# Kernel tuning notes

Hardware: AMD Instinct MI355X
Metric: run time of the kernel (lower is better)

The kernel has to match this reference:

```python
import jax, jax.numpy as jnp
import numpy as np

B, P, K, H, C = 8, 4096, 20, 64, 40  # clouds, points/cloud, knn k, hidden_feat, num_classes
NEG = 0.2  # LeakyReLU negative slope used by the repo MLP


def setup_inputs() -> dict:
    key = jax.random.key(0)
    ks = jax.random.split(key, 16)
    w = lambda k, shape: (jax.random.normal(k, shape, jnp.float32) / np.sqrt(shape[0]))
    return {
        "x": jax.random.normal(ks[0], (B * P, 3), jnp.float32),
        "batch": jnp.repeat(jnp.arange(B, dtype=jnp.int32), P),
        "W1": w(ks[1], (2 * 3, H)), "b1": jnp.zeros((H,), jnp.float32),
        "W2": w(ks[2], (2 * H, H)), "b2": jnp.zeros((H,), jnp.float32),
        "W3": w(ks[3], (2 * H, H)), "b3": jnp.zeros((H,), jnp.float32),
        "Wl": w(ks[4], (3 * H, 1024)), "bl": jnp.zeros((1024,), jnp.float32),
        "Wm1": w(ks[5], (1024, 256)), "bm1": jnp.zeros((256,), jnp.float32),
        "Wm2": w(ks[6], (256, 128)), "bm2": jnp.zeros((128,), jnp.float32),
        "Wo": w(ks[7], (128, C)), "bo": jnp.zeros((C,), jnp.float32),
    }


def _knn_idx(x):
    # x: [B,P,d] -> indices of K nearest neighbors (excluding self): [B,P,K]
    d2 = jnp.sum(x * x, axis=-1)  # [B,P]
    dist = d2[:, :, None] + d2[:, None, :] - 2.0 * jnp.einsum('bpd,bqd->bpq', x, x)
    dist = dist + jnp.eye(x.shape[1], dtype=x.dtype) * 1e10  # mask self-loops
    return jax.lax.top_k(-dist, K)[1]


def _edge_conv(x, W, b):
    # DynamicEdgeConv with max aggregation: nn([x_i, x_j - x_i]) maxed over K neighbors
    idx = _knn_idx(x)                                    # [B,P,K]
    x_j = jax.vmap(lambda xb, ib: xb[ib])(x, idx)        # [B,P,K,d]
    x_i = jnp.broadcast_to(x[:, :, None, :], x_j.shape)  # [B,P,K,d]
    feat = jnp.concatenate([x_i, x_j - x_i], axis=-1)    # [B,P,K,2d]
    h = jax.nn.leaky_relu(feat @ W + b, NEG)             # [B,P,K,H]
    return jnp.max(h, axis=2)                            # [B,P,H]


def reference(x, batch, W1, b1, W2, b2, W3, b3, Wl, bl, Wm1, bm1, Wm2, bm2, Wo, bo):
    # batch is sorted with equal-size clouds -> reshape to [B,P,3]
    xb = x.reshape(B, P, 3)
    x1 = _edge_conv(xb, W1, b1)
    x2 = _edge_conv(x1, W2, b2)
    x3 = _edge_conv(x2, W3, b3)
    h = jnp.concatenate([x1, x2, x3], axis=-1)           # [B,P,3H]
    h = jax.nn.leaky_relu(h @ Wl + bl, NEG)
    h = jax.nn.leaky_relu(h @ Wm1 + bm1, NEG)            # dropout = identity (eval)
    h = jax.nn.leaky_relu(h @ Wm2 + bm2, NEG)
    out = h @ Wo + bo                                    # [B,P,C]
    return jax.nn.log_softmax(out, axis=-1).reshape(B * P, C)
```

## Files before the change

### kernel.cpp

```cpp
#include <hip/hip_runtime.h>
#include <cstddef>
#include <cstdint>

constexpr int B_ = 8, P_ = 4096, K_ = 20, H_ = 64, C_ = 40;
constexpr int NPT = B_ * P_;
#define NEG_SLOPE 0.2f

typedef unsigned long long u64;
typedef unsigned int u32;
typedef unsigned short u16;
typedef __attribute__((ext_vector_type(8))) short bf16x8;
typedef __attribute__((ext_vector_type(4))) float f32x4;

__device__ inline u16 f2bf(float v) {
    u32 bits = __float_as_uint(v);
    return (u16)((bits + 0x7FFFu + ((bits >> 16) & 1)) >> 16);
}
__device__ inline float bf2f(u16 h) { return __uint_as_float((u32)h << 16); }

__device__ __forceinline__ void bubble20f(float (&a)[K_], float key) {
    float carry = key;
#pragma unroll
    for (int s = 0; s < K_; ++s) {
        float as = a[s];
        a[s]  = fminf(carry, as);
        carry = fmaxf(carry, as);
    }
}
__device__ __forceinline__ float mkkey(float dist, int cid) {
    return __uint_as_float((__float_as_uint(dist) & 0xFFFFF000u) | (u32)cid);
}

__global__ __launch_bounds__(256) void pack4_kernel(const float* __restrict__ x,
                                                    float4* __restrict__ xp) {
    int i = blockIdx.x * 256 + threadIdx.x;
    if (i >= NPT) return;
    float ax = x[(size_t)i * 3], ay = x[(size_t)i * 3 + 1], az = x[(size_t)i * 3 + 2];
    xp[i] = make_float4(ax, ay, az, ax * ax + ay * ay + az * az);
}

__global__ __launch_bounds__(256) void d2cvt2_kernel(const float* __restrict__ x,
                                                     float* __restrict__ d2,
                                                     u16* __restrict__ xh,
                                                     u16* __restrict__ xm) {
    int i = blockIdx.x * 256 + threadIdx.x;
    if (i >= NPT) return;
    const float* r = x + (size_t)i * 64;
    float s = 0.f;
#pragma unroll
    for (int d8 = 0; d8 < 64; d8 += 8) {
        float4 v0 = *(const float4*)(r + d8);
        float4 v1 = *(const float4*)(r + d8 + 4);
        s += v0.x * v0.x + v0.y * v0.y + v0.z * v0.z + v0.w * v0.w;
        s += v1.x * v1.x + v1.y * v1.y + v1.z * v1.z + v1.w * v1.w;
        float av[8] = {v0.x, v0.y, v0.z, v0.w, v1.x, v1.y, v1.z, v1.w};
        bf16x8 vh, vm;
#pragma unroll
        for (int j = 0; j < 8; ++j) {
            u16 h = f2bf(av[j]);
            float r1 = av[j] - bf2f(h);
            vh[j] = (short)h; vm[j] = (short)f2bf(r1);
        }
        *(bf16x8*)(xh + (size_t)i * 64 + d8) = vh;
        *(bf16x8*)(xm + (size_t)i * 64 + d8) = vm;
    }
    d2[i] = s;
}

__global__ __launch_bounds__(256) void knnf3_kernel(const float4* __restrict__ xp,
                                                    int* __restrict__ idx) {
    int b = blockIdx.y;
    int q0 = blockIdx.x * 64;
    const float4* xb = xp + (size_t)b * P_;

    int t = threadIdx.x, w = t >> 6, ln = t & 63;
    int q  = ln & 15;
    int ss = ln >> 4;

    int qrow = q0 + w * 16 + q;
    float4 qv = xb[qrow];

    float a[K_];
#pragma unroll
    for (int s = 0; s < K_; ++s)
        a[s] = __uint_as_float(0x7F7FF000u | (u32)s);
    const float PINV = __uint_as_float(0x7F800000u);
    const float BIGF = __uint_as_float(0x7F7FFFFFu);

    float p0 = PINV, p1 = PINV, p2 = PINV, p3 = PINV;
    int pcnt = 0;
    float kthr = BIGF;

#pragma unroll 1
    for (int c0 = 0; c0 < P_; c0 += 64) {
#pragma unroll
        for (int nt = 0; nt < 4; ++nt) {
            float4 cv[4];
#pragma unroll
            for (int r = 0; r < 4; ++r)
                cv[r] = xb[c0 + nt * 16 + ss * 4 + r];
#pragma unroll
            for (int r = 0; r < 4; ++r) {
                int cID = c0 + nt * 16 + ss * 4 + r;
                float dv = (qv.w + cv[r].w)
                         - 2.f * (qv.x * cv[r].x + qv.y * cv[r].y + qv.z * cv[r].z);
                if (cID == qrow) dv += 1e10f;
                dv = fmaxf(dv, 0.f);
                if (__any(dv <= kthr)) {
                    float key = mkkey(dv, cID);
                    bool pass = key < a[K_ - 1];
                    p3 = pass ? p2 : p3;
                    p2 = pass ? p1 : p2;
                    p1 = pass ? p0 : p1;
                    p0 = pass ? key : p0;
                    pcnt = pass ? pcnt + 1 : pcnt;
                    if (__any(pcnt >= 4)) {
                        bubble20f(a, p3); bubble20f(a, p2); bubble20f(a, p1); bubble20f(a, p0);
                        p0 = p1 = p2 = p3 = PINV; pcnt = 0;
                        kthr = __uint_as_float(__float_as_uint(a[K_ - 1]) | 0xFFFu);
                    }
                }
            }
        }
    }
    bubble20f(a, p3); bubble20f(a, p2); bubble20f(a, p1); bubble20f(a, p0);

    int* op = idx + ((size_t)(b * P_ + qrow)) * K_;
#pragma unroll 1
    for (int k = 0; k < K_; ++k) {
        float v = a[0];
        float v1 = __shfl_xor(v, 16);
        v = fminf(v, v1);
        float v2 = __shfl_xor(v, 32);
        v = fminf(v, v2);
        bool win = (__float_as_uint(a[0]) == __float_as_uint(v));
#pragma unroll
        for (int s = 0; s < K_ - 1; ++s) a[s] = win ? a[s + 1] : a[s];
        a[K_ - 1] = win ? BIGF : a[K_ - 1];
        if (ss == 0)
            op[k] = b * P_ + (int)(__float_as_uint(v) & 0xFFFu);
    }
}

__global__ __launch_bounds__(256) void knnm64_kernel(const u16* __restrict__ xh,
                                                     const u16* __restrict__ xm,
                                                     const float* __restrict__ d2,
                                                     int* __restrict__ idx) {
    __shared__ u16 sH[64 * 64];
    __shared__ u16 sM[64 * 64];
    __shared__ float sd2[P_];

    int b = blockIdx.y;
    int q0 = blockIdx.x * 64;
    const u16* xhb = xh + (size_t)b * P_ * 64;
    const u16* xmb = xm + (size_t)b * P_ * 64;
    const float* d2b = d2 + (size_t)b * P_;

    int t = threadIdx.x, w = t >> 6, ln = t & 63;
    int q  = ln & 15;
    int ss = ln >> 4;

    for (int i = t; i < P_ / 4; i += 256)
        ((float4*)sd2)[i] = ((const float4*)d2b)[i];

    int qrow = q0 + w * 16 + q;
    bf16x8 qh[2], qm[2];
#pragma unroll
    for (int kt = 0; kt < 2; ++kt) {
        size_t off = (size_t)qrow * 64 + kt * 32 + ss * 8;
        qh[kt] = *(const bf16x8*)(xhb + off);
        qm[kt] = *(const bf16x8*)(xmb + off);
    }

    __syncthreads();
    float qd2 = sd2[qrow];

    float a[K_];
#pragma unroll
    for (int s = 0; s < K_; ++s)
        a[s] = __uint_as_float(0x7F7FF000u | (u32)s);
    const float PINV = __uint_as_float(0x7F800000u);
    const float BIGF = __uint_as_float(0x7F7FFFFFu);

    float p0 = PINV, p1 = PINV, p2 = PINV, p3 = PINV;
    int pcnt = 0;
    float kthr = BIGF;

    int sr = t >> 2;
    int sk2 = (t & 3) * 32;
    int sbase = sr * 128, sswz = (sr & 7) << 4;
    size_t sgof = (size_t)sr * 64 + (t & 3) * 16;

#pragma unroll 1
    for (int c0 = 0; c0 < P_; c0 += 64) {
        __syncthreads();
        {
            size_t g = (size_t)c0 * 64 + sgof;
            bf16x8 h0 = *(const bf16x8*)(xhb + g);
            bf16x8 h1 = *(const bf16x8*)(xhb + g + 8);
            bf16x8 m0 = *(const bf16x8*)(xmb + g);
            bf16x8 m1 = *(const bf16x8*)(xmb + g + 8);
            *(bf16x8*)((char*)sH + sbase + (sk2 ^ sswz)) = h0;
            *(bf16x8*)((char*)sH + sbase + ((sk2 + 16) ^ sswz)) = h1;
            *(bf16x8*)((char*)sM + sbase + (sk2 ^ sswz)) = m0;
            *(bf16x8*)((char*)sM + sbase + ((sk2 + 16) ^ sswz)) = m1;
        }
        __syncthreads();

        f32x4 acc[4];
#pragma unroll
        for (int nt = 0; nt < 4; ++nt) {
            acc[nt] = (f32x4){0.f, 0.f, 0.f, 0.f};
            int r = nt * 16 + q;
            int base = r * 128, swz = (r & 7) << 4;
#pragma unroll
            for (int kt = 0; kt < 2; ++kt) {
                int k2 = kt * 64 + ss * 16;
                bf16x8 ch = *(const bf16x8*)((char*)sH + base + (k2 ^ swz));
                bf16x8 cm = *(const bf16x8*)((char*)sM + base + (k2 ^ swz));
                acc[nt] = __builtin_amdgcn_mfma_f32_16x16x32_bf16(cm, qh[kt], acc[nt], 0, 0, 0);
                acc[nt] = __builtin_amdgcn_mfma_f32_16x16x32_bf16(ch, qm[kt], acc[nt], 0, 0, 0);
                acc[nt] = __builtin_amdgcn_mfma_f32_16x16x32_bf16(ch, qh[kt], acc[nt], 0, 0, 0);
            }
        }

        float dvv[4][4];
        float mn = 3.4e38f;
#pragma unroll
        for (int nt = 0; nt < 4; ++nt) {
#pragma unroll
            for (int r = 0; r < 4; ++r) {
                int cID = c0 + nt * 16 + ss * 4 + r;
                float dv = (qd2 + sd2[cID]) - 2.f * acc[nt][r];
                if (cID == qrow) dv += 1e10f;
                dv = fmaxf(dv, 0.f);
                dvv[nt][r] = dv;
                mn = fminf(mn, dv);
            }
        }
        if (__any(mn <= kthr)) {
#pragma unroll
            for (int nt = 0; nt < 4; ++nt) {
#pragma unroll
                for (int r = 0; r < 4; ++r) {
                    float dv = dvv[nt][r];
                    if (__any(dv <= kthr)) {
                        float key = mkkey(dv, c0 + nt * 16 + ss * 4 + r);
                        bool pass = key < a[K_ - 1];
                        p3 = pass ? p2 : p3;
                        p2 = pass ? p1 : p2;
                        p1 = pass ? p0 : p1;
                        p0 = pass ? key : p0;
                        pcnt = pass ? pcnt + 1 : pcnt;
                        if (__any(pcnt >= 4)) {
                            bubble20f(a, p3); bubble20f(a, p2); bubble20f(a, p1); bubble20f(a, p0);
                            p0 = p1 = p2 = p3 = PINV; pcnt = 0;
                            kthr = __uint_as_float(__float_as_uint(a[K_ - 1]) | 0xFFFu);
                        }
                    }
                }
            }
        }
    }
    bubble20f(a, p3); bubble20f(a, p2); bubble20f(a, p1); bubble20f(a, p0);

    int* op = idx + ((size_t)(b * P_ + qrow)) * K_;
#pragma unroll 1
    for (int k = 0; k < K_; ++k) {
        float v = a[0];
        float v1 = __shfl_xor(v, 16);
        v = fminf(v, v1);
        float v2 = __shfl_xor(v, 32);
        v = fminf(v, v2);
        bool win = (__float_as_uint(a[0]) == __float_as_uint(v));
#pragma unroll
        for (int s = 0; s < K_ - 1; ++s) a[s] = win ? a[s + 1] : a[s];
        a[K_ - 1] = win ? BIGF : a[K_ - 1];
        if (ss == 0)
            op[k] = b * P_ + (int)(__float_as_uint(v) & 0xFFFu);
    }
}

__global__ __launch_bounds__(256) void prep_kernel(const float* __restrict__ W2,
                                                   const float* __restrict__ b2,
                                                   const float* __restrict__ W3,
                                                   const float* __restrict__ b3,
                                                   const float* __restrict__ Wl,
                                                   const float* __restrict__ Wm1,
                                                   const float* __restrict__ Wm2,
                                                   float* __restrict__ Wpk2, float* __restrict__ bpk2,
                                                   float* __restrict__ Wpk3, float* __restrict__ bpk3,
                                                   u16* __restrict__ WlT,
                                                   u16* __restrict__ Wm1T,
                                                   u16* __restrict__ Wm2T) {
    int t = blockIdx.x * 256 + threadIdx.x;
    if (t < 8192) {
        int d = t >> 7, h2 = t & 127;
        Wpk2[t] = (h2 < 64) ? W2[d * 64 + h2] : W2[(64 + d) * 64 + (h2 - 64)];
        if (t < 128) bpk2[t] = (t < 64) ? b2[t] : 0.f;
    } else if (t < 16384) {
        int t2 = t - 8192;
        int d = t2 >> 7, h2 = t2 & 127;
        Wpk3[t2] = (h2 < 64) ? W3[d * 64 + h2] : W3[(64 + d) * 64 + (h2 - 64)];
        if (t2 < 128) bpk3[t2] = (t2 < 64) ? b3[t2] : 0.f;
    } else if (t < 212992) {
        int t2 = t - 16384;
        int k = t2 >> 10, n = t2 & 1023;
        WlT[(size_t)n * 192 + k] = f2bf(Wl[t2]);
    } else if (t < 475136) {
        int t2 = t - 212992;
        int k = t2 >> 8, n = t2 & 255;
        Wm1T[(size_t)n * 1024 + k] = f2bf(Wm1[t2]);
    } else if (t < 507904) {
        int t2 = t - 475136;
        int k = t2 >> 7, n = t2 & 127;
        Wm2T[(size_t)n * 256 + k] = f2bf(Wm2[t2]);
    }
}

__global__ __launch_bounds__(256) void uv3_kernel(const float* __restrict__ x,
                                                  const float* __restrict__ W,
                                                  const float* __restrict__ b,
                                                  float* __restrict__ UV) {
    int t = blockIdx.x * 256 + threadIdx.x;
    int p = t >> 7, h2 = t & 127;
    float x0 = x[p * 3], x1 = x[p * 3 + 1], x2 = x[p * 3 + 2];
    float r;
    if (h2 < 64) {
        r = b[h2] + x0 * W[h2] + x1 * W[64 + h2] + x2 * W[128 + h2];
    } else {
        int h = h2 - 64;
        r = x0 * W[192 + h] + x1 * W[256 + h] + x2 * W[320 + h];
    }
    UV[t] = r;
}

__global__ __launch_bounds__(256) void edgemax_kernel(const float* __restrict__ UV,
                                                      const int* __restrict__ idx,
                                                      float* __restrict__ xout) {
    int wv = threadIdx.x >> 6, lane = threadIdx.x & 63;
    int p = blockIdx.x * 4 + wv;
    const float* uvp = UV + (size_t)p * 128;
    float duv = uvp[lane] - uvp[64 + lane];
    const int* ip = idx + (size_t)p * K_;
    int jj[K_];
#pragma unroll
    for (int k = 0; k < K_; ++k) jj[k] = ip[k];
    float m = -3.4e38f;
#pragma unroll
    for (int k = 0; k < K_; ++k) {
        float vj = UV[(size_t)jj[k] * 128 + 64 + lane];
        float t = duv + vj;
        m = fmaxf(m, fmaxf(t, NEG_SLOPE * t));
    }
    xout[(size_t)p * H_ + lane] = m;
}

__global__ __launch_bounds__(256) void gemm_kernel(const float* __restrict__ A1,
                                                   const float* __restrict__ Wm,
                                                   const float* __restrict__ bias,
                                                   float* __restrict__ Cm,
                                                   int M, int N, int Kd, int leaky) {
    __shared__ float sA[32][68];
    __shared__ float sB[32][68];

    int tid = threadIdx.x;
    int row0 = blockIdx.x * 64, col0 = blockIdx.y * 64;
    int tx = tid & 15, ty = tid >> 4;

    int lr  = tid >> 2;
    int lk4 = (tid & 3) * 4;
    int lkb = tid >> 4;
    int lnb = (tid & 15) * 4;

    float acc[4][4] = {};

    for (int k0 = 0; k0 < Kd; k0 += 32) {
        int arow = row0 + lr;
#pragma unroll
        for (int h = 0; h < 32; h += 16) {
            int kk = k0 + lk4 + h;
            const float* src = A1 + (size_t)arow * Kd + kk;
            float4 av = *(const float4*)src;
            sA[lk4 + h + 0][lr] = av.x; sA[lk4 + h + 1][lr] = av.y;
            sA[lk4 + h + 2][lr] = av.z; sA[lk4 + h + 3][lr] = av.w;
        }
        int bcol = col0 + lnb;
#pragma unroll
        for (int h = 0; h < 32; h += 16) {
            float4 bv = make_float4(0.f, 0.f, 0.f, 0.f);
            if (bcol < N) bv = *(const float4*)(Wm + (size_t)(k0 + lkb + h) * N + bcol);
            *(float4*)&sB[lkb + h][lnb] = bv;
        }
        __syncthreads();

#pragma unroll
        for (int kk2 = 0; kk2 < 32; ++kk2) {
            float4 a = *(const float4*)&sA[kk2][ty * 4];
            float4 bb = *(const float4*)&sB[kk2][tx * 4];
            acc[0][0] = fmaf(a.x, bb.x, acc[0][0]); acc[0][1] = fmaf(a.x, bb.y, acc[0][1]);
            acc[0][2] = fmaf(a.x, bb.z, acc[0][2]); acc[0][3] = fmaf(a.x, bb.w, acc[0][3]);
            acc[1][0] = fmaf(a.y, bb.x, acc[1][0]); acc[1][1] = fmaf(a.y, bb.y, acc[1][1]);
            acc[1][2] = fmaf(a.y, bb.z, acc[1][2]); acc[1][3] = fmaf(a.y, bb.w, acc[1][3]);
            acc[2][0] = fmaf(a.z, bb.x, acc[2][0]); acc[2][1] = fmaf(a.z, bb.y, acc[2][1]);
            acc[2][2] = fmaf(a.z, bb.z, acc[2][2]); acc[2][3] = fmaf(a.z, bb.w, acc[2][3]);
            acc[3][0] = fmaf(a.w, bb.x, acc[3][0]); acc[3][1] = fmaf(a.w, bb.y, acc[3][1]);
            acc[3][2] = fmaf(a.w, bb.z, acc[3][2]); acc[3][3] = fmaf(a.w, bb.w, acc[3][3]);
        }
        __syncthreads();
    }

    for (int i = 0; i < 4; ++i) {
        int row = row0 + ty * 4 + i;
        for (int j = 0; j < 4; ++j) {
            int col = col0 + tx * 4 + j;
            if (col < N) {
                float v = acc[i][j] + bias[col];
                if (leaky) v = v > 0.f ? v : NEG_SLOPE * v;
                Cm[(size_t)row * N + col] = v;
            }
        }
    }
}

template <int KD, int OUT_BF16>
__global__ __launch_bounds__(256) void gemm_mfma_kernel(const u16* __restrict__ A,
                                                        const u16* __restrict__ BT,
                                                        const float* __restrict__ bias,
                                                        void* __restrict__ Cout,
                                                        int N, int leaky) {
    __shared__ u16 sA[128 * 64];
    __shared__ u16 sB[128 * 64];

    int t = threadIdx.x;
    int wave = t >> 6, lane = t & 63;
    int wm = wave >> 1, wn = wave & 1;
    int row0 = blockIdx.x * 128;
    int col0 = blockIdx.y * 128;

    f32x4 acc[4][4] = {};

    for (int k0 = 0; k0 < KD; k0 += 64) {
        __syncthreads();
#pragma unroll
        for (int i = 0; i < 4; ++i) {
            int li = t + i * 256;
            int r = li >> 3;
            int kc = (li & 7) * 8;
            bf16x8 v = *(const bf16x8*)(A + (size_t)(row0 + r) * KD + k0 + kc);
            *(bf16x8*)((char*)sA + r * 128 + ((kc * 2) ^ ((r & 7) << 4))) = v;
        }
#pragma unroll
        for (int i = 0; i < 4; ++i) {
            int li = t + i * 256;
            int n = li >> 3;
            int kc = (li & 7) * 8;
            bf16x8 v = *(const bf16x8*)(BT + (size_t)(col0 + n) * KD + k0 + kc);
            *(bf16x8*)((char*)sB + n * 128 + ((kc * 2) ^ ((n & 7) << 4))) = v;
        }
        __syncthreads();

#pragma unroll
        for (int kk = 0; kk < 2; ++kk) {
            int kb = kk * 64 + (lane >> 4) * 16;
            bf16x8 af[4], bfr[4];
#pragma unroll
            for (int mi = 0; mi < 4; ++mi) {
                int r = wm * 64 + mi * 16 + (lane & 15);
                af[mi] = *(const bf16x8*)((char*)sA + r * 128 + (kb ^ ((r & 7) << 4)));
            }
#pragma unroll
            for (int ni = 0; ni < 4; ++ni) {
                int n = wn * 64 + ni * 16 + (lane & 15);
                bfr[ni] = *(const bf16x8*)((char*)sB + n * 128 + (kb ^ ((n & 7) << 4)));
            }
#pragma unroll
            for (int mi = 0; mi < 4; ++mi)
#pragma unroll
                for (int ni = 0; ni < 4; ++ni)
                    acc[mi][ni] = __builtin_amdgcn_mfma_f32_16x16x32_bf16(
                        af[mi], bfr[ni], acc[mi][ni], 0, 0, 0);
        }
    }

#pragma unroll
    for (int ni = 0; ni < 4; ++ni) {
        int col = col0 + wn * 64 + ni * 16 + (lane & 15);
        float bs = bias[col];
#pragma unroll
        for (int mi = 0; mi < 4; ++mi) {
#pragma unroll
            for (int r = 0; r < 4; ++r) {
                int row = row0 + wm * 64 + mi * 16 + (lane >> 4) * 4 + r;
                float v = acc[mi][ni][r] + bs;
                if (leaky) v = v > 0.f ? v : NEG_SLOPE * v;
                if (OUT_BF16)
                    ((u16*)Cout)[(size_t)row * N + col] = f2bf(v);
                else
                    ((float*)Cout)[(size_t)row * N + col] = v;
            }
        }
    }
}

__global__ __launch_bounds__(256) void gemm_mfma_cat_kernel(const float* __restrict__ x1,
                                                            const float* __restrict__ x2,
                                                            const float* __restrict__ x3,
                                                            const u16* __restrict__ BT,
                                                            const float* __restrict__ bias,
                                                            u16* __restrict__ Cout,
                                                            int N) {
    __shared__ u16 sA[128 * 64];
    __shared__ u16 sB[128 * 64];

    int t = threadIdx.x;
    int wave = t >> 6, lane = t & 63;
    int wm = wave >> 1, wn = wave & 1;
    int row0 = blockIdx.x * 128;
    int col0 = blockIdx.y * 128;

    f32x4 acc[4][4] = {};

#pragma unroll 1
    for (int k0 = 0; k0 < 192; k0 += 64) {
        const float* src = (k0 == 0) ? x1 : (k0 == 64) ? x2 : x3;
        __syncthreads();
#pragma unroll
        for (int i = 0; i < 4; ++i) {
            int li = t + i * 256;
            int r = li >> 3;
            int kc = (li & 7) * 8;
            const float* sp = src + (size_t)(row0 + r) * 64 + kc;
            float4 a0 = *(const float4*)sp;
            float4 a1 = *(const float4*)(sp + 4);
            bf16x8 v;
            v[0] = (short)f2bf(a0.x); v[1] = (short)f2bf(a0.y);
            v[2] = (short)f2bf(a0.z); v[3] = (short)f2bf(a0.w);
            v[4] = (short)f2bf(a1.x); v[5] = (short)f2bf(a1.y);
            v[6] = (short)f2bf(a1.z); v[7] = (short)f2bf(a1.w);
            *(bf16x8*)((char*)sA + r * 128 + ((kc * 2) ^ ((r & 7) << 4))) = v;
        }
#pragma unroll
        for (int i = 0; i < 4; ++i) {
            int li = t + i * 256;
            int n = li >> 3;
            int kc = (li & 7) * 8;
            bf16x8 v = *(const bf16x8*)(BT + (size_t)(col0 + n) * 192 + k0 + kc);
            *(bf16x8*)((char*)sB + n * 128 + ((kc * 2) ^ ((n & 7) << 4))) = v;
        }
        __syncthreads();

#pragma unroll
        for (int kk = 0; kk < 2; ++kk) {
            int kb = kk * 64 + (lane >> 4) * 16;
            bf16x8 af[4], bfr[4];
#pragma unroll
            for (int mi = 0; mi < 4; ++mi) {
                int r = wm * 64 + mi * 16 + (lane & 15);
                af[mi] = *(const bf16x8*)((char*)sA + r * 128 + (kb ^ ((r & 7) << 4)));
            }
#pragma unroll
            for (int ni = 0; ni < 4; ++ni) {
                int n = wn * 64 + ni * 16 + (lane & 15);
                bfr[ni] = *(const bf16x8*)((char*)sB + n * 128 + (kb ^ ((n & 7) << 4)));
            }
#pragma unroll
            for (int mi = 0; mi < 4; ++mi)
#pragma unroll
                for (int ni = 0; ni < 4; ++ni)
                    acc[mi][ni] = __builtin_amdgcn_mfma_f32_16x16x32_bf16(
                        af[mi], bfr[ni], acc[mi][ni], 0, 0, 0);
        }
    }

#pragma unroll
    for (int ni = 0; ni < 4; ++ni) {
        int col = col0 + wn * 64 + ni * 16 + (lane & 15);
        float bs = bias[col];
#pragma unroll
        for (int mi = 0; mi < 4; ++mi) {
#pragma unroll
            for (int r = 0; r < 4; ++r) {
                int row = row0 + wm * 64 + mi * 16 + (lane >> 4) * 4 + r;
                float v = acc[mi][ni][r] + bs;
                v = v > 0.f ? v : NEG_SLOPE * v;
                Cout[(size_t)row * N + col] = f2bf(v);
            }
        }
    }
}

__global__ __launch_bounds__(256) void lsm_wo_kernel(const float* __restrict__ act3,
                                                     const float* __restrict__ Wo,
                                                     const float* __restrict__ bo,
                                                     float* __restrict__ out) {
    __shared__ float sWo[128 * 44];
    __shared__ float sAct[4][128];

    int t = threadIdx.x;
    for (int i = t; i < 128 * 40; i += 256) {
        int k = i / 40, c = i % 40;
        sWo[k * 44 + c] = Wo[i];
    }
    __syncthreads();

    int wv = t >> 6, lane = t & 63;
    int row = blockIdx.x * 4 + wv;
    sAct[wv][lane]      = act3[(size_t)row * 128 + lane];
    sAct[wv][64 + lane] = act3[(size_t)row * 128 + 64 + lane];

    float acc = (lane < C_) ? bo[lane] : -3.4e38f;
    if (lane < C_) {
#pragma unroll 8
        for (int k = 0; k < 128; ++k)
            acc = fmaf(sAct[wv][k], sWo[k * 44 + lane], acc);
    }
    float m = acc;
#pragma unroll
    for (int s = 1; s < 64; s <<= 1) m = fmaxf(m, __shfl_xor(m, s));
    float e = (lane < C_) ? expf(acc - m) : 0.f;
    float sum = e;
#pragma unroll
    for (int s = 1; s < 64; s <<= 1) sum += __shfl_xor(sum, s);
    if (lane < C_) out[(size_t)row * C_ + lane] = acc - m - logf(sum);
}

extern "C" void kernel_launch(void* const* d_in, const int* in_sizes, int n_in,
                              void* d_out, int out_size, void* d_ws, size_t ws_size,
                              hipStream_t stream) {
    const float* x   = (const float*)d_in[0];
    const float* W1  = (const float*)d_in[2];
    const float* b1  = (const float*)d_in[3];
    const float* W2  = (const float*)d_in[4];
    const float* b2  = (const float*)d_in[5];
    const float* W3  = (const float*)d_in[6];
    const float* b3  = (const float*)d_in[7];
    const float* Wl  = (const float*)d_in[8];
    const float* bl  = (const float*)d_in[9];
    const float* Wm1 = (const float*)d_in[10];
    const float* bm1 = (const float*)d_in[11];
    const float* Wm2 = (const float*)d_in[12];
    const float* bm2 = (const float*)d_in[13];
    const float* Wo  = (const float*)d_in[14];
    const float* bo  = (const float*)d_in[15];
    float* out = (float*)d_out;

    char* ws = (char*)d_ws;
    float* x1   = (float*)(ws);
    float* x2   = (float*)(ws + 8388608);
    float* x3   = (float*)(ws + 16777216);
    int*   idx  = (int*)  (ws + 25165824);
    float* d2   = (float*)(ws + 27787264);
    char* hb = ws + 27918336;
    float4* xp  = (float4*)(hb);
    u16*   xhs  = (u16*)(hb);
    u16*   xms  = (u16*)(hb + 4194304);
    float* UV   = (float*)(hb);
    float* Wpk2 = (float*)(ws + 44695552);
    float* bpk2 = (float*)(ws + 44728320);
    float* Wpk3 = (float*)(ws + 44728832);
    float* bpk3 = (float*)(ws + 44761600);
    u16*   WlT  = (u16*)  (ws + 44762112);
    u16*   Wm1T = (u16*)  (ws + 45155328);
    u16*   Wm2T = (u16*)  (ws + 45679616);
    u16*   act1 = (u16*)(hb);
    u16*   act2 = (u16*)(ws + 45745152);
    float* act3 = (float*)(hb);

    prep_kernel<<<1984, 256, 0, stream>>>(W2, b2, W3, b3, Wl, Wm1, Wm2,
                                          Wpk2, bpk2, Wpk3, bpk3, WlT, Wm1T, Wm2T);

    pack4_kernel<<<NPT / 256, 256, 0, stream>>>(x, xp);
    knnf3_kernel<<<dim3(P_ / 64, B_), 256, 0, stream>>>(xp, idx);
    uv3_kernel<<<NPT * 128 / 256, 256, 0, stream>>>(x, W1, b1, UV);
    edgemax_kernel<<<NPT / 4, 256, 0, stream>>>(UV, idx, x1);
    d2cvt2_kernel<<<NPT / 256, 256, 0, stream>>>(x1, d2, xhs, xms);
    knnm64_kernel<<<dim3(P_ / 64, B_), 256, 0, stream>>>(xhs, xms, d2, idx);
    gemm_kernel<<<dim3(NPT / 64, 2), 256, 0, stream>>>(x1, Wpk2, bpk2, UV, NPT, 128, 64, 0);
    edgemax_kernel<<<NPT / 4, 256, 0, stream>>>(UV, idx, x2);
    d2cvt2_kernel<<<NPT / 256, 256, 0, stream>>>(x2, d2, xhs, xms);
    knnm64_kernel<<<dim3(P_ / 64, B_), 256, 0, stream>>>(xhs, xms, d2, idx);
    gemm_kernel<<<dim3(NPT / 64, 2), 256, 0, stream>>>(x2, Wpk3, bpk3, UV, NPT, 128, 64, 0);
    edgemax_kernel<<<NPT / 4, 256, 0, stream>>>(UV, idx, x3);

    for (int c = 0; c < 4; ++c) {
        size_t r0 = (size_t)c * 8192;
        gemm_mfma_cat_kernel<<<dim3(64, 8), 256, 0, stream>>>(x1 + r0 * 64, x2 + r0 * 64,
                                                              x3 + r0 * 64, WlT, bl, act1, 1024);
        gemm_mfma_kernel<1024, 1><<<dim3(64, 2), 256, 0, stream>>>(act1, Wm1T, bm1, act2, 256, 1);
        gemm_mfma_kernel<256, 0><<<dim3(64, 1), 256, 0, stream>>>(act2, Wm2T, bm2, act3, 128, 1);
        lsm_wo_kernel<<<2048, 256, 0, stream>>>(act3, Wo, bo, out + r0 * C_);
    }
}
```

Baseline: 880.1 us.

## Split KNN candidate range across two wave groups and merge top-K in LDS

Both KNN kernels now launch 512 threads per block, and each half of the waves scans half of the candidate points for the same 64 queries. Each group writes its sorted top-20 keys to shared memory, and one wave merges the two lists into the final neighbor indices. The aim is to double parallelism per query block so the serial candidate scan is shorter and latency is better hidden, since the grid has only 512 blocks. In exchange there is a serial 20-step merge, more shared memory and registers per block, and possible occupancy limits at 512 threads.

```diff
diff --git a/kernel.cpp b/kernel.cpp
--- a/kernel.cpp
+++ b/kernel.cpp
@@ -4,6 +4,7 @@
 
 constexpr int B_ = 8, P_ = 4096, K_ = 20, H_ = 64, C_ = 40;
 constexpr int NPT = B_ * P_;
+constexpr int HALF = P_ / 2;
 #define NEG_SLOPE 0.2f
 
 typedef unsigned long long u64;
@@ -67,17 +68,20 @@
     d2[i] = s;
 }
 
-__global__ __launch_bounds__(256) void knnf3_kernel(const float4* __restrict__ xp,
+__global__ __launch_bounds__(512) void knnf3_kernel(const float4* __restrict__ xp,
                                                     int* __restrict__ idx) {
+    __shared__ float sKeys[2][64][21];
+
     int b = blockIdx.y;
     int q0 = blockIdx.x * 64;
     const float4* xb = xp + (size_t)b * P_;
 
-    int t = threadIdx.x, w = t >> 6, ln = t & 63;
+    int t = threadIdx.x, wave = t >> 6, ln = t & 63;
+    int g = wave >> 2, w2 = wave & 3;
     int q  = ln & 15;
     int ss = ln >> 4;
 
-    int qrow = q0 + w * 16 + q;
+    int qrow = q0 + w2 * 16 + q;
     float4 qv = xb[qrow];
 
     float a[K_];
@@ -91,8 +95,9 @@
     int pcnt = 0;
     float kthr = BIGF;
 
+    int cbase = g * HALF;
 #pragma unroll 1
-    for (int c0 = 0; c0 < P_; c0 += 64) {
+    for (int c0 = cbase; c0 < cbase + HALF; c0 += 64) {
 #pragma unroll
         for (int nt = 0; nt < 4; ++nt) {
             float4 cv[4];
@@ -125,7 +130,6 @@
     }
     bubble20f(a, p3); bubble20f(a, p2); bubble20f(a, p1); bubble20f(a, p0);
 
-    int* op = idx + ((size_t)(b * P_ + qrow)) * K_;
 #pragma unroll 1
     for (int k = 0; k < K_; ++k) {
         float v = a[0];
@@ -137,18 +141,35 @@
 #pragma unroll
         for (int s = 0; s < K_ - 1; ++s) a[s] = win ? a[s + 1] : a[s];
         a[K_ - 1] = win ? BIGF : a[K_ - 1];
-        if (ss == 0)
+        if (ss == 0) sKeys[g][w2 * 16 + q][k] = v;
+    }
+    __syncthreads();
+
+    if (t < 64) {
+        int qq = t;
+        int* op = idx + ((size_t)(b * P_ + q0 + qq)) * K_;
+        int iA = 0, iB = 0;
+#pragma unroll 1
+        for (int k = 0; k < K_; ++k) {
+            float va = sKeys[0][qq][iA];
+            float vb = sKeys[1][qq][iB];
+            bool ta = va < vb;
+            float v = ta ? va : vb;
+            iA += ta ? 1 : 0;
+            iB += ta ? 0 : 1;
             op[k] = b * P_ + (int)(__float_as_uint(v) & 0xFFFu);
-    }
-}
-
-__global__ __launch_bounds__(256) void knnm64_kernel(const u16* __restrict__ xh,
+        }
+    }
+}
+
+__global__ __launch_bounds__(512) void knnm64_kernel(const u16* __restrict__ xh,
                                                      const u16* __restrict__ xm,
                                                      const float* __restrict__ d2,
                                                      int* __restrict__ idx) {
-    __shared__ u16 sH[64 * 64];
-    __shared__ u16 sM[64 * 64];
+    __shared__ u16 sH[2][64 * 64];
+    __shared__ u16 sM[2][64 * 64];
     __shared__ float sd2[P_];
+    __shared__ float sKeys[2][64][21];
 
     int b = blockIdx.y;
     int q0 = blockIdx.x * 64;
@@ -156,14 +177,15 @@
     const u16* xmb = xm + (size_t)b * P_ * 64;
     const float* d2b = d2 + (size_t)b * P_;
 
-    int t = threadIdx.x, w = t >> 6, ln = t & 63;
+    int t = threadIdx.x, wave = t >> 6, ln = t & 63;
+    int g = wave >> 2, w2 = wave & 3;
     int q  = ln & 15;
     int ss = ln >> 4;
 
-    for (int i = t; i < P_ / 4; i += 256)
+    for (int i = t; i < P_ / 4; i += 512)
         ((float4*)sd2)[i] = ((const float4*)d2b)[i];
 
-    int qrow = q0 + w * 16 + q;
+    int qrow = q0 + w2 * 16 + q;
     bf16x8 qh[2], qm[2];
 #pragma unroll
     for (int kt = 0; kt < 2; ++kt) {
@@ -186,26 +208,35 @@
     int pcnt = 0;
     float kthr = BIGF;
 
-    int sr = t >> 2;
+    int srow = t >> 2;
+    int sbuf = srow >> 6;
+    int sr = srow & 63;
     int sk2 = (t & 3) * 32;
     int sbase = sr * 128, sswz = (sr & 7) << 4;
     size_t sgof = (size_t)sr * 64 + (t & 3) * 16;
 
 #pragma unroll 1
-    for (int c0 = 0; c0 < P_; c0 += 64) {
+    for (int it = 0; it < HALF / 64; ++it) {
+        int c0A = it * 64;
+        int c0B = HALF + it * 64;
         __syncthreads();
         {
-            size_t g = (size_t)c0 * 64 + sgof;
-            bf16x8 h0 = *(const bf16x8*)(xhb + g);
-            bf16x8 h1 = *(const bf16x8*)(xhb + g + 8);
-            bf16x8 m0 = *(const bf16x8*)(xmb + g);
-            bf16x8 m1 = *(const bf16x8*)(xmb + g + 8);
-            *(bf16x8*)((char*)sH + sbase + (sk2 ^ sswz)) = h0;
-            *(bf16x8*)((char*)sH + sbase + ((sk2 + 16) ^ sswz)) = h1;
-            *(bf16x8*)((char*)sM + sbase + (sk2 ^ sswz)) = m0;
-            *(bf16x8*)((char*)sM + sbase + ((sk2 + 16) ^ sswz)) = m1;
+            int cc0 = sbuf ? c0B : c0A;
+            size_t gaddr = (size_t)cc0 * 64 + sgof;
+            bf16x8 h0 = *(const bf16x8*)(xhb + gaddr);
+            bf16x8 h1 = *(const bf16x8*)(xhb + gaddr + 8);
+            bf16x8 m0 = *(const bf16x8*)(xmb + gaddr);
+            bf16x8 m1 = *(const bf16x8*)(xmb + gaddr + 8);
+            *(bf16x8*)((char*)sH[sbuf] + sbase + (sk2 ^ sswz)) = h0;
+            *(bf16x8*)((char*)sH[sbuf] + sbase + ((sk2 + 16) ^ sswz)) = h1;
+            *(bf16x8*)((char*)sM[sbuf] + sbase + (sk2 ^ sswz)) = m0;
+            *(bf16x8*)((char*)sM[sbuf] + sbase + ((sk2 + 16) ^ sswz)) = m1;
         }
         __syncthreads();
+
+        int cg = g ? c0B : c0A;
+        const char* bH = (const char*)sH[g];
+        const char* bM = (const char*)sM[g];
 
         f32x4 acc[4];
 #pragma unroll
@@ -216,8 +247,8 @@
 #pragma unroll
             for (int kt = 0; kt < 2; ++kt) {
                 int k2 = kt * 64 + ss * 16;
-                bf16x8 ch = *(const bf16x8*)((char*)sH + base + (k2 ^ swz));
-                bf16x8 cm = *(const bf16x8*)((char*)sM + base + (k2 ^ swz));
+                bf16x8 ch = *(const bf16x8*)(bH + base + (k2 ^ swz));
+                bf16x8 cm = *(const bf16x8*)(bM + base + (k2 ^ swz));
                 acc[nt] = __builtin_amdgcn_mfma_f32_16x16x32_bf16(cm, qh[kt], acc[nt], 0, 0, 0);
                 acc[nt] = __builtin_amdgcn_mfma_f32_16x16x32_bf16(ch, qm[kt], acc[nt], 0, 0, 0);
                 acc[nt] = __builtin_amdgcn_mfma_f32_16x16x32_bf16(ch, qh[kt], acc[nt], 0, 0, 0);
@@ -230,7 +261,7 @@
         for (int nt = 0; nt < 4; ++nt) {
 #pragma unroll
             for (int r = 0; r < 4; ++r) {
-                int cID = c0 + nt * 16 + ss * 4 + r;
+                int cID = cg + nt * 16 + ss * 4 + r;
                 float dv = (qd2 + sd2[cID]) - 2.f * acc[nt][r];
                 if (cID == qrow) dv += 1e10f;
                 dv = fmaxf(dv, 0.f);
@@ -245,7 +276,7 @@
                 for (int r = 0; r < 4; ++r) {
                     float dv = dvv[nt][r];
                     if (__any(dv <= kthr)) {
-                        float key = mkkey(dv, c0 + nt * 16 + ss * 4 + r);
+                        float key = mkkey(dv, cg + nt * 16 + ss * 4 + r);
                         bool pass = key < a[K_ - 1];
                         p3 = pass ? p2 : p3;
                         p2 = pass ? p1 : p2;
@@ -264,7 +295,6 @@
     }
     bubble20f(a, p3); bubble20f(a, p2); bubble20f(a, p1); bubble20f(a, p0);
 
-    int* op = idx + ((size_t)(b * P_ + qrow)) * K_;
 #pragma unroll 1
     for (int k = 0; k < K_; ++k) {
         float v = a[0];
@@ -276,8 +306,24 @@
 #pragma unroll
         for (int s = 0; s < K_ - 1; ++s) a[s] = win ? a[s + 1] : a[s];
         a[K_ - 1] = win ? BIGF : a[K_ - 1];
-        if (ss == 0)
+        if (ss == 0) sKeys[g][w2 * 16 + q][k] = v;
+    }
+    __syncthreads();
+
+    if (t < 64) {
+        int qq = t;
+        int* op = idx + ((size_t)(b * P_ + q0 + qq)) * K_;
+        int iA = 0, iB = 0;
+#pragma unroll 1
+        for (int k = 0; k < K_; ++k) {
+            float va = sKeys[0][qq][iA];
+            float vb = sKeys[1][qq][iB];
+            bool ta = va < vb;
+            float v = ta ? va : vb;
+            iA += ta ? 1 : 0;
+            iB += ta ? 0 : 1;
             op[k] = b * P_ + (int)(__float_as_uint(v) & 0xFFFu);
+        }
     }
 }
 
@@ -671,15 +717,15 @@
                                           Wpk2, bpk2, Wpk3, bpk3, WlT, Wm1T, Wm2T);
 
     pack4_kernel<<<NPT / 256, 256, 0, stream>>>(x, xp);
-    knnf3_kernel<<<dim3(P_ / 64, B_), 256, 0, stream>>>(xp, idx);
+    knnf3_kernel<<<dim3(P_ / 64, B_), 512, 0, stream>>>(xp, idx);
     uv3_kernel<<<NPT * 128 / 256, 256, 0, stream>>>(x, W1, b1, UV);
     edgemax_kernel<<<NPT / 4, 256, 0, stream>>>(UV, idx, x1);
     d2cvt2_kernel<<<NPT / 256, 256, 0, stream>>>(x1, d2, xhs, xms);
-    knnm64_kernel<<<dim3(P_ / 64, B_), 256, 0, stream>>>(xhs, xms, d2, idx);
+    knnm64_kernel<<<dim3(P_ / 64, B_), 512, 0, stream>>>(xhs, xms, d2, idx);
     gemm_kernel<<<dim3(NPT / 64, 2), 256, 0, stream>>>(x1, Wpk2, bpk2, UV, NPT, 128, 64, 0);
     edgemax_kernel<<<NPT / 4, 256, 0, stream>>>(UV, idx, x2);
     d2cvt2_kernel<<<NPT / 256, 256, 0, stream>>>(x2, d2, xhs, xms);
-    knnm64_kernel<<<dim3(P_ / 64, B_), 256, 0, stream>>>(xhs, xms, d2, idx);
+    knnm64_kernel<<<dim3(P_ / 64, B_), 512, 0, stream>>>(xhs, xms, d2, idx);
     gemm_kernel<<<dim3(NPT / 64, 2), 256, 0, stream>>>(x2, Wpk3, bpk3, UV, NPT, 128, 64, 0);
     edgemax_kernel<<<NPT / 4, 256, 0, stream>>>(UV, idx, x3);
 
```

Result: no change. 871.9 us (-0.9%).
